# Optimization experiments

Measured on AMD Instinct MI355X. Metric: run time of the kernel, lower is better.

The kernel has to match this reference:

```python
import jax, jax.numpy as jnp
import numpy as np

N, D = 16384, 32          # nodes, max neighbors
IN_F, HID, OUT_F = 128, 128, 128
HEADS = 8
HD = HID // HEADS         # head dim
TDIM = 64                 # Time2Vec dim
NORM = float(np.sqrt(1.0 / HD))


def _lin_params(key, fan_in, fan_out):
    k1, k2 = jax.random.split(key)
    lim = 1.0 / np.sqrt(fan_in)
    W = jax.random.uniform(k1, (fan_in, fan_out), jnp.float32, -lim, lim)
    b = jax.random.uniform(k2, (fan_out,), jnp.float32, -lim, lim)
    return W, b


def setup_inputs() -> dict:
    key = jax.random.key(0)
    ks = jax.random.split(key, 16)
    x = jax.random.normal(ks[0], (N, IN_F), jnp.float32)
    neighbors = jax.random.randint(ks[1], (N, D), 0, N)
    times = jax.random.uniform(ks[2], (N, D), jnp.float32)
    t = jax.random.uniform(ks[3], (1,), jnp.float32)
    # node KQV
    Wk, bk = _lin_params(ks[4], IN_F, HID)
    Wq, bq = _lin_params(ks[5], IN_F, HID)
    Wv, bv = _lin_params(ks[6], IN_F, HID)
    # Time2Vec kernel: [w0*t+b0, sin(t*W + B)] -> TDIM feats
    w0 = jax.random.normal(ks[7], (1,), jnp.float32)
    b0 = jax.random.normal(ks[8], (1,), jnp.float32)
    Wt = jax.random.normal(ks[9], (1, TDIM - 1), jnp.float32)
    Bt = jax.random.normal(ks[10], (TDIM - 1,), jnp.float32)
    # time KQV
    Wtk, btk = _lin_params(ks[11], TDIM, HID)
    Wtq, btq = _lin_params(ks[12], TDIM, HID)
    Wtv, btv = _lin_params(ks[13], TDIM, HID)
    # output MLP
    W1, b1 = _lin_params(ks[14], HID + IN_F, HID)
    W2, b2 = _lin_params(ks[15], HID, OUT_F)
    return dict(x=x, neighbors=neighbors, times=times, t=t,
                Wk=Wk, bk=bk, Wq=Wq, bq=bq, Wv=Wv, bv=bv,
                w0=w0, b0=b0, Wt=Wt, Bt=Bt,
                Wtk=Wtk, btk=btk, Wtq=Wtq, btq=btq, Wtv=Wtv, btv=btv,
                W1=W1, b1=b1, W2=W2, b2=b2)


def _t2v(ts, w0, b0, Wt, Bt):
    # ts: [..., 1] -> [..., TDIM]
    return jnp.concatenate([ts * w0 + b0, jnp.sin(ts @ Wt + Bt)], axis=-1)


def reference(x, neighbors, times, t,
              Wk, bk, Wq, bq, Wv, bv,
              w0, b0, Wt, Bt,
              Wtk, btk, Wtq, btq, Wtv, btv,
              W1, b1, W2, b2):
    t0 = t[0]
    # node-level K/Q/V for all nodes
    k_ = x @ Wk + bk
    q_ = x @ Wq + bq
    v_ = x @ Wv + bv
    # time encodings
    enc_t = _t2v(t.reshape(1, 1), w0, b0, Wt, Bt)          # [1, TDIM]
    tq = enc_t @ Wtq + btq                                  # [1, HID] (same for every target node)
    enc_nb = _t2v(times[..., None], w0, b0, Wt, Bt)        # [N, D, TDIM]
    tk = enc_nb @ Wtk + btk                                 # [N, D, HID]
    tv = enc_nb @ Wtv + btv
    # gather neighbor K/V and add time encodings
    q = q_ + tq                                             # [N, HID]
    k = k_[neighbors] + tk                                  # [N, D, HID]
    v = v_[neighbors] + tv
    # multi-head attention over (time-masked) neighbors
    qh = q.reshape(N, HEADS, HD)
    kh = k.reshape(N, D, HEADS, HD)
    vh = v.reshape(N, D, HEADS, HD)
    scores = jnp.einsum('nhd,nmhd->nhm', qh, kh) * NORM     # [N, H, D]
    mask = times <= t0                                      # [N, D]
    scores = jnp.where(mask[:, None, :], scores, -1e9)
    attn = jax.nn.softmax(scores, axis=-1)
    h = jnp.einsum('nhm,nmhd->nhd', attn, vh).reshape(N, HID)
    # nodes with no valid (time <= t) neighbors output zeros
    h = jnp.where(mask.any(axis=-1)[:, None], h, 0.0)
    # output MLP on [x || h]
    z = jnp.concatenate([x, h], axis=1)
    return jax.nn.relu(z @ W1 + b1) @ W2 + b2
```

## Files before the change

kernel.cpp:

```cpp
#include <hip/hip_runtime.h>
#include <hip/hip_bf16.h>

#define NNODES 16384

typedef unsigned short u16;
typedef unsigned int   u32;
typedef __attribute__((ext_vector_type(8))) short bf16x8;
typedef __attribute__((ext_vector_type(4))) float f32x4;

__device__ __forceinline__ float bfl(u32 u) { return __uint_as_float(u << 16); }
__device__ __forceinline__ float bfh(u32 u) { return __uint_as_float(u & 0xffff0000u); }
__device__ __forceinline__ u16 f2b(float f) {
    u32 u = __float_as_uint(f);
    return (u16)((u + 0x7fffu + ((u >> 16) & 1u)) >> 16);
}
__device__ __forceinline__ u32 pk2(float a, float b) {
    return (u32)f2b(a) | ((u32)f2b(b) << 16);
}
__device__ __forceinline__ bf16x8 bcast8(int4 v) {
    return __builtin_bit_cast(bf16x8, v);
}

#if defined(__has_builtin)
#if __has_builtin(__builtin_amdgcn_fdot2_f32_bf16)
#define HAVE_DOT2 1
#endif
#endif
#ifndef HAVE_DOT2
#define HAVE_DOT2 0
#endif

#if HAVE_DOT2
typedef __attribute__((ext_vector_type(2))) __bf16 bf16x2;
__device__ __forceinline__ float dot2b(u32 a, u32 b, float c) {
    return __builtin_amdgcn_fdot2_f32_bf16(__builtin_bit_cast(bf16x2, a),
                                           __builtin_bit_cast(bf16x2, b), c, false);
}
#else
__device__ __forceinline__ float dot2b(u32 a, u32 b, float c) {
    return c + bfl(a) * bfl(b) + bfh(a) * bfh(b);
}
#endif

__global__ __launch_bounds__(256) void setup_all(
    const float* __restrict__ Wk, const float* __restrict__ Wq,
    const float* __restrict__ Wv, const float* __restrict__ W1,
    const float* __restrict__ W2,
    const float* __restrict__ t,  const float* __restrict__ bq,
    const float* __restrict__ btq,const float* __restrict__ Wtq,
    const float* __restrict__ w0, const float* __restrict__ b0,
    const float* __restrict__ Wt, const float* __restrict__ Bt,
    const float* __restrict__ Wtk,const float* __restrict__ Wtv,
    u16* __restrict__ Wts, float* __restrict__ qbias,
    float* __restrict__ gb, u32* __restrict__ Wtvp, u16* __restrict__ WGt)
{
    __shared__ float sb[128 * 17 + 64 * 17];
    int b = blockIdx.x, tt = threadIdx.x;

    if (b < 96) {
        int mat = b >> 4, tile = b & 15;
        const float* src = (mat == 0) ? Wk : (mat == 1) ? Wq : (mat == 2) ? Wv
                         : (mat == 3) ? W1 : (mat == 4) ? (W1 + 128 * 128) : W2;
        u16* dst = Wts + (size_t)mat * 16384;
        #pragma unroll
        for (int i = 0; i < 4; i++) {
            int o = i * 256 + tt;
            int cl = o >> 7, k = o & 127;
            int c = tile * 8 + cl;
            dst[c * 128 + k] = f2b(src[k * 128 + c]);
        }
    } else if (b == 96 || b == 97) {
        float tv = t[0];
        if (tt < 64)
            sb[tt] = (tt == 0) ? (w0[0] * tv + b0[0])
                               : __sinf(tv * Wt[tt - 1] + Bt[tt - 1]);
        __syncthreads();
        if (tt < 128) {
            float s = bq[tt] + btq[tt];
            for (int k = 0; k < 64; k++)
                s += sb[k] * Wtq[k * 128 + tt];
            sb[64 + tt] = s;
            if (b == 96) qbias[tt] = s;
        }
        __syncthreads();
        if (b == 97) {
            #pragma unroll
            for (int r = 0; r < 2; r++) {
                int hj = tt + r * 256;
                int h = hj >> 6, j = hj & 63;
                float s = 0.f;
                #pragma unroll
                for (int d = 0; d < 16; d++)
                    s += sb[64 + h * 16 + d] * Wtk[(size_t)j * 128 + h * 16 + d];
                gb[hj] = s;
            }
        }
    } else if (b == 98) {
        #pragma unroll
        for (int i = 0; i < 16; i++) {
            int idx = i * 256 + tt;
            int kp = idx >> 7, c = idx & 127;
            Wtvp[idx] = pk2(Wtv[(size_t)(2 * kp) * 128 + c],
                            Wtv[(size_t)(2 * kp + 1) * 128 + c]);
        }
    } else {
        int h = b - 99;
        float* WqL  = sb;
        float* WtkL = sb + 128 * 17;
        #pragma unroll
        for (int i = 0; i < 8; i++) {
            int o = i * 256 + tt;
            int k = o >> 4, d = o & 15;
            WqL[k * 17 + d] = Wq[(size_t)k * 128 + h * 16 + d];
        }
        #pragma unroll
        for (int i = 0; i < 4; i++) {
            int o = i * 256 + tt;
            int j = o >> 4, d = o & 15;
            WtkL[j * 17 + d] = Wtk[(size_t)j * 128 + h * 16 + d];
        }
        __syncthreads();
        int j = tt >> 2, kb = (tt & 3) * 32;
        float wk[16];
        #pragma unroll
        for (int d = 0; d < 16; d++) wk[d] = WtkL[j * 17 + d];
        u32 out[16];
        #pragma unroll
        for (int kk2 = 0; kk2 < 16; kk2++) {
            int k = kb + 2 * kk2;
            float s0 = 0.f, s1 = 0.f;
            #pragma unroll
            for (int d = 0; d < 16; d++) {
                s0 += WqL[k * 17 + d] * wk[d];
                s1 += WqL[(k + 1) * 17 + d] * wk[d];
            }
            out[kk2] = pk2(s0, s1);
        }
        int4* dst = (int4*)(WGt + (size_t)(h * 64 + j) * 128 + kb);
        const int4* srcv = (const int4*)out;
        #pragma unroll
        for (int i = 0; i < 4; i++) dst[i] = srcv[i];
    }
}

__global__ __launch_bounds__(256) void gemm8m2(
    const float* __restrict__ x, const u16* __restrict__ Wts,
    const u16* __restrict__ WGt,
    const float* __restrict__ bk, const float* __restrict__ qbias,
    const float* __restrict__ bv, const float* __restrict__ b1,
    const float* __restrict__ gb,
    u16* __restrict__ Kb, u16* __restrict__ Qb,
    u16* __restrict__ Vb, u16* __restrict__ Pb, u16* __restrict__ Gb)
{
    __shared__ u16 As[128 * 128];
    __shared__ u16 Ws[128 * 128];
    int t = threadIdx.x;
    int rb = blockIdx.x * 128;
    int pair = blockIdx.y;

    u32* As32 = (u32*)As;
    u32* Ws32 = (u32*)Ws;
    const float2* Ap = (const float2*)(x + (size_t)rb * 128);
    #pragma unroll
    for (int i = 0; i < 32; i++) {
        int idx2 = i * 256 + t;
        int r = idx2 >> 6, k2 = idx2 & 63;
        float2 v = Ap[idx2];
        As32[(r * 64 + k2) ^ ((r & 7) << 2)] = pk2(v.x, v.y);
    }

    int wid = t >> 6, lane = t & 63;
    int l15 = lane & 15, lg = lane >> 4;
    int mb = wid * 32;
    int xo = (l15 & 7) << 3;

    #pragma unroll
    for (int half = 0; half < 2; half++) {
        int mat = pair + half * 4;
        const u16* Wt = (mat < 4) ? (Wts + (size_t)mat * 16384)
                                  : (WGt + (size_t)(mat - 4) * 16384);
        const float* bias = (mat == 0) ? bk : (mat == 1) ? qbias
                          : (mat == 2) ? bv : (mat == 3) ? b1
                          : (gb + (mat - 4) * 128);
        const u32* Wp = (const u32*)Wt;
        #pragma unroll
        for (int i = 0; i < 32; i++) {
            int idx2 = i * 256 + t;
            int c = idx2 >> 6, k2 = idx2 & 63;
            Ws32[(c * 64 + k2) ^ ((c & 7) << 2)] = Wp[idx2];
        }
        __syncthreads();

        f32x4 acc[2][8];
        #pragma unroll
        for (int mi = 0; mi < 2; mi++)
            #pragma unroll
            for (int nt = 0; nt < 8; nt++)
                acc[mi][nt] = (f32x4){0.f, 0.f, 0.f, 0.f};

        #pragma unroll
        for (int ks = 0; ks < 4; ks++) {
            int kq = ks * 32 + lg * 8;
            bf16x8 a0 = *(bf16x8*)&As[((mb + l15) * 128 + kq) ^ xo];
            bf16x8 a1 = *(bf16x8*)&As[((mb + 16 + l15) * 128 + kq) ^ xo];
            #pragma unroll
            for (int nt = 0; nt < 8; nt++) {
                bf16x8 b = *(bf16x8*)&Ws[((nt * 16 + l15) * 128 + kq) ^ xo];
                acc[0][nt] = __builtin_amdgcn_mfma_f32_16x16x32_bf16(a0, b, acc[0][nt], 0, 0, 0);
                acc[1][nt] = __builtin_amdgcn_mfma_f32_16x16x32_bf16(a1, b, acc[1][nt], 0, 0, 0);
            }
        }

        u16* dst = (mat == 0) ? Kb : (mat == 1) ? Qb : (mat == 2) ? Vb
                 : (mat == 3) ? Pb : Gb;
        #pragma unroll
        for (int mi = 0; mi < 2; mi++) {
            #pragma unroll
            for (int nt = 0; nt < 8; nt++) {
                int c = nt * 16 + l15;
                float bvv = bias[c];
                #pragma unroll
                for (int j = 0; j < 4; j++) {
                    size_t row = rb + mb + mi * 16 + lg * 4 + j;
                    float v = acc[mi][nt][j] + bvv;
                    if (mat < 4) dst[row * 128 + c] = f2b(v);
                    else         dst[row * 512 + (size_t)(mat - 4) * 128 + c] = f2b(v);
                }
            }
        }
        __syncthreads();
    }
}

__global__ __launch_bounds__(256) void mlp_fused(
    const u16* __restrict__ Hb, const u16* __restrict__ Wts,
    const u16* __restrict__ Pb, const float* __restrict__ b2,
    float* __restrict__ out)
{
    __shared__ u16 As[64 * 128];
    __shared__ u16 Ws[128 * 128];
    int t = threadIdx.x;
    int rb = blockIdx.x * 64;
    u32* As32 = (u32*)As;
    u32* Ws32 = (u32*)Ws;

    const u32* Hp = (const u32*)(Hb + (size_t)rb * 128);
    #pragma unroll
    for (int i = 0; i < 16; i++) {
        int idx2 = i * 256 + t;
        int r = idx2 >> 6, k2 = idx2 & 63;
        As32[(r * 64 + k2) ^ ((r & 7) << 2)] = Hp[idx2];
    }
    {
        const u32* Wp = (const u32*)(Wts + 4 * 16384);
        #pragma unroll
        for (int i = 0; i < 32; i++) {
            int idx2 = i * 256 + t;
            int c = idx2 >> 6, k2 = idx2 & 63;
            Ws32[(c * 64 + k2) ^ ((c & 7) << 2)] = Wp[idx2];
        }
    }
    __syncthreads();

    int wid = t >> 6, lane = t & 63;
    int l15 = lane & 15, lg = lane >> 4;
    int mb = wid * 16;
    int xo = (l15 & 7) << 3;

    f32x4 acc[8];
    #pragma unroll
    for (int nt = 0; nt < 8; nt++) acc[nt] = (f32x4){0.f, 0.f, 0.f, 0.f};
    #pragma unroll
    for (int ks = 0; ks < 4; ks++) {
        int kq = ks * 32 + lg * 8;
        bf16x8 a0 = *(bf16x8*)&As[((mb + l15) * 128 + kq) ^ xo];
        #pragma unroll
        for (int nt = 0; nt < 8; nt++) {
            bf16x8 b = *(bf16x8*)&Ws[((nt * 16 + l15) * 128 + kq) ^ xo];
            acc[nt] = __builtin_amdgcn_mfma_f32_16x16x32_bf16(a0, b, acc[nt], 0, 0, 0);
        }
    }
    __syncthreads();

    #pragma unroll
    for (int nt = 0; nt < 8; nt++) {
        int c = nt * 16 + l15;
        #pragma unroll
        for (int j = 0; j < 4; j++) {
            int row = mb + lg * 4 + j;
            float pv = bfl((u32)Pb[(size_t)(rb + row) * 128 + c]);
            float v = fmaxf(acc[nt][j] + pv, 0.f);
            As[(row * 128 + c) ^ ((row & 7) << 3)] = f2b(v);
        }
    }
    {
        const u32* Wp = (const u32*)(Wts + 5 * 16384);
        #pragma unroll
        for (int i = 0; i < 32; i++) {
            int idx2 = i * 256 + t;
            int c = idx2 >> 6, k2 = idx2 & 63;
            Ws32[(c * 64 + k2) ^ ((c & 7) << 2)] = Wp[idx2];
        }
    }
    __syncthreads();

    #pragma unroll
    for (int nt = 0; nt < 8; nt++) acc[nt] = (f32x4){0.f, 0.f, 0.f, 0.f};
    #pragma unroll
    for (int ks = 0; ks < 4; ks++) {
        int kq = ks * 32 + lg * 8;
        bf16x8 a0 = *(bf16x8*)&As[((mb + l15) * 128 + kq) ^ xo];
        #pragma unroll
        for (int nt = 0; nt < 8; nt++) {
            bf16x8 b = *(bf16x8*)&Ws[((nt * 16 + l15) * 128 + kq) ^ xo];
            acc[nt] = __builtin_amdgcn_mfma_f32_16x16x32_bf16(a0, b, acc[nt], 0, 0, 0);
        }
    }
    #pragma unroll
    for (int nt = 0; nt < 8; nt++) {
        int c = nt * 16 + l15;
        float bvv = b2[c];
        #pragma unroll
        for (int j = 0; j < 4; j++) {
            size_t row = rb + mb + lg * 4 + j;
            out[row * 128 + c] = acc[nt][j] + bvv;
        }
    }
}

__global__ __launch_bounds__(256, 5) void attn_kernel(
    const int*   __restrict__ neighbors, const float* __restrict__ times,
    const float* __restrict__ tptr,
    const u16* __restrict__ Kb, const u16* __restrict__ Qb,
    const u16* __restrict__ Vb, const u16* __restrict__ Gb,
    const float* __restrict__ btk,  const u32* __restrict__ Wtvp,
    const float* __restrict__ btv,
    const float* __restrict__ w0,   const float* __restrict__ b0,
    const float* __restrict__ Wt,   const float* __restrict__ Bt,
    u16* __restrict__ Hb)
{
    __shared__ u16   enc[4][32][72];
    __shared__ u32   gbp[4][8][32];
    __shared__ u32   qb[4][64];
    __shared__ float pbuf[4][8][33];
    __shared__ u16   ewp[4][8][66];
    __shared__ int   nbb[4][32];
    __shared__ float cb_[4][8];

    int t = threadIdx.x;
    int wid = t >> 6, lane = t & 63;
    int n = blockIdx.x * 4 + wid;
    float t0 = tptr[0];
    int l15 = lane & 15, lg = lane >> 4;

    qb[wid][lane] = ((const u32*)Qb)[(size_t)n * 64 + lane];
    {
        int4 g4 = *(const int4*)((const u32*)Gb + (size_t)n * 256 + 4 * lane);
        const u32* gw = (const u32*)&g4;
        #pragma unroll
        for (int i = 0; i < 4; i++) {
            int q4 = 4 * lane + i;
            gbp[wid][q4 >> 5][q4 & 31] = gw[i];
        }
    }

    int m = lane & 31, h2 = lane >> 5;
    if (lane < 32) nbb[wid][lane] = neighbors[n * 32 + lane];
    float tm = times[n * 32 + m];
    bool valid = (tm <= t0);
    unsigned long long bal = __ballot(valid);
    bool anyv = (bal != 0ull);

    u32 vpre[32];
    #pragma unroll
    for (int mm = 0; mm < 32; mm++) {
        int nbm = nbb[wid][mm];
        vpre[mm] = *(const u32*)(Vb + (size_t)nbm * 128 + 2 * lane);
    }

    float W0 = w0[0], B0 = b0[0];
    int kbase = 32 * h2;
    #pragma unroll
    for (int i = 0; i < 16; i++) {
        int k0 = kbase + 2 * i;
        float v0 = (k0 == 0) ? (W0 * tm + B0) : __sinf(tm * Wt[k0 - 1] + Bt[k0 - 1]);
        float v1 = __sinf(tm * Wt[k0] + Bt[k0]);
        *(u32*)&enc[wid][m][k0] = pk2(v0, v1);
    }

    if (lane < 8) {
        float s = 0.f;
        #pragma unroll
        for (int j = 0; j < 8; j++) {
            u32 qp = qb[wid][lane * 8 + j];
            s += bfl(qp) * btk[lane * 16 + 2 * j] + bfh(qp) * btk[lane * 16 + 2 * j + 1];
        }
        cb_[wid][lane] = s;
    }

    f32x4 accS[2];
    accS[0] = (f32x4){0.f, 0.f, 0.f, 0.f};
    accS[1] = (f32x4){0.f, 0.f, 0.f, 0.f};

    int nb0 = nbb[wid][l15];
    int nb1 = nbb[wid][l15 + 16];
    const u16* K0 = Kb + (size_t)nb0 * 128;
    const u16* K1 = Kb + (size_t)nb1 * 128;
    const int4 zero4 = {0, 0, 0, 0};
    #pragma unroll
    for (int ks = 0; ks < 4; ks++) {
        bf16x8 qf = bcast8((l15 == ks * 2 + (lg >> 1))
                               ? *(const int4*)&qb[wid][ks * 16 + lg * 4]
                               : zero4);
        bf16x8 k0f = bcast8(*(const int4*)(K0 + ks * 32 + lg * 8));
        bf16x8 k1f = bcast8(*(const int4*)(K1 + ks * 32 + lg * 8));
        accS[0] = __builtin_amdgcn_mfma_f32_16x16x32_bf16(k0f, qf, accS[0], 0, 0, 0);
        accS[1] = __builtin_amdgcn_mfma_f32_16x16x32_bf16(k1f, qf, accS[1], 0, 0, 0);
    }
    #pragma unroll
    for (int ks = 0; ks < 2; ks++) {
        int4 gi = zero4;
        if (l15 < 8) {
            int2 ga = *(const int2*)&gbp[wid][l15][ks * 16 + lg * 4];
            int2 gbq = *(const int2*)&gbp[wid][l15][ks * 16 + lg * 4 + 2];
            gi.x = ga.x; gi.y = ga.y; gi.z = gbq.x; gi.w = gbq.y;
        }
        bf16x8 gf = bcast8(gi);
        bf16x8 e0 = *(const bf16x8*)&enc[wid][l15][ks * 32 + lg * 8];
        bf16x8 e1 = *(const bf16x8*)&enc[wid][l15 + 16][ks * 32 + lg * 8];
        accS[0] = __builtin_amdgcn_mfma_f32_16x16x32_bf16(e0, gf, accS[0], 0, 0, 0);
        accS[1] = __builtin_amdgcn_mfma_f32_16x16x32_bf16(e1, gf, accS[1], 0, 0, 0);
    }

    float cbv = (l15 < 8) ? cb_[wid][l15] : 0.f;
    float sc[2][4];
    #pragma unroll
    for (int mt = 0; mt < 2; mt++) {
        #pragma unroll
        for (int j = 0; j < 4; j++) {
            int mr = mt * 16 + lg * 4 + j;
            float v = 0.25f * (accS[mt][j] + cbv);
            sc[mt][j] = ((bal >> mr) & 1ull) ? v : -1e9f;
        }
    }
    float mx = sc[0][0];
    #pragma unroll
    for (int mt = 0; mt < 2; mt++)
        #pragma unroll
        for (int j = 0; j < 4; j++) mx = fmaxf(mx, sc[mt][j]);
    mx = fmaxf(mx, __shfl_xor(mx, 16));
    mx = fmaxf(mx, __shfl_xor(mx, 32));
    float p[2][4];
    float s = 0.f;
    #pragma unroll
    for (int mt = 0; mt < 2; mt++)
        #pragma unroll
        for (int j = 0; j < 4; j++) { p[mt][j] = __expf(sc[mt][j] - mx); s += p[mt][j]; }
    s += __shfl_xor(s, 16);
    s += __shfl_xor(s, 32);
    float inv = 1.0f / s;
    if (l15 < 8) {
        #pragma unroll
        for (int mt = 0; mt < 2; mt++)
            #pragma unroll
            for (int j = 0; j < 4; j++)
                pbuf[wid][l15][mt * 16 + lg * 4 + j] = p[mt][j] * inv;
    }

    {
        int hh = l15 & 7;
        float pa[8];
        #pragma unroll
        for (int j = 0; j < 8; j++) pa[j] = pbuf[wid][hh][8 * lg + j];
        int4 ai;
        ai.x = pk2(pa[0], pa[1]); ai.y = pk2(pa[2], pa[3]);
        ai.z = pk2(pa[4], pa[5]); ai.w = pk2(pa[6], pa[7]);
        bf16x8 af = bcast8(ai);
        #pragma unroll
        for (int nt = 0; nt < 4; nt++) {
            int col = nt * 16 + l15;
            int4 bi;
            bi.x = (u32)enc[wid][8 * lg + 0][col] | ((u32)enc[wid][8 * lg + 1][col] << 16);
            bi.y = (u32)enc[wid][8 * lg + 2][col] | ((u32)enc[wid][8 * lg + 3][col] << 16);
            bi.z = (u32)enc[wid][8 * lg + 4][col] | ((u32)enc[wid][8 * lg + 5][col] << 16);
            bi.w = (u32)enc[wid][8 * lg + 6][col] | ((u32)enc[wid][8 * lg + 7][col] << 16);
            bf16x8 bfr = bcast8(bi);
            f32x4 ce = (f32x4){0.f, 0.f, 0.f, 0.f};
            ce = __builtin_amdgcn_mfma_f32_16x16x32_bf16(af, bfr, ce, 0, 0, 0);
            if (lg < 2) {
                #pragma unroll
                for (int j = 0; j < 4; j++)
                    ewp[wid][4 * lg + j][col] = f2b(ce[j]);
            }
        }
    }

    int myh = lane >> 3;
    float av0 = 0.f, av1 = 0.f;
    #pragma unroll
    for (int mm = 0; mm < 32; mm++) {
        float a = pbuf[wid][myh][mm];
        av0 += a * bfl(vpre[mm]);
        av1 += a * bfh(vpre[mm]);
    }
    float ht0 = 0.f, ht1 = 0.f;
    #pragma unroll 8
    for (int kp = 0; kp < 32; kp++) {
        u32 ew = *(const u32*)&ewp[wid][myh][2 * kp];
        int2 wv = *(const int2*)&Wtvp[kp * 128 + 2 * lane];
        ht0 = dot2b(ew, (u32)wv.x, ht0);
        ht1 = dot2b(ew, (u32)wv.y, ht1);
    }
    float2 bt2 = *(const float2*)&btv[2 * lane];
    float ox = anyv ? (av0 + ht0 + bt2.x) : 0.0f;
    float oy = anyv ? (av1 + ht1 + bt2.y) : 0.0f;
    ((u32*)Hb)[(size_t)n * 64 + lane] = pk2(ox, oy);
}

extern "C" void kernel_launch(void* const* d_in, const int* in_sizes, int n_in,
                              void* d_out, int out_size, void* d_ws, size_t ws_size,
                              hipStream_t stream)
{
    const float* x        = (const float*)d_in[0];
    const int*   neighbors= (const int*)  d_in[1];
    const float* times    = (const float*)d_in[2];
    const float* t        = (const float*)d_in[3];
    const float* Wk  = (const float*)d_in[4];
    const float* bk  = (const float*)d_in[5];
    const float* Wq  = (const float*)d_in[6];
    const float* bq  = (const float*)d_in[7];
    const float* Wv  = (const float*)d_in[8];
    const float* bv  = (const float*)d_in[9];
    const float* w0  = (const float*)d_in[10];
    const float* b0  = (const float*)d_in[11];
    const float* Wt  = (const float*)d_in[12];
    const float* Bt  = (const float*)d_in[13];
    const float* Wtk = (const float*)d_in[14];
    const float* btk = (const float*)d_in[15];
    const float* Wtq = (const float*)d_in[16];
    const float* btq = (const float*)d_in[17];
    const float* Wtv = (const float*)d_in[18];
    const float* btv = (const float*)d_in[19];
    const float* W1  = (const float*)d_in[20];
    const float* b1  = (const float*)d_in[21];
    const float* W2  = (const float*)d_in[22];
    const float* b2  = (const float*)d_in[23];

    float* ws = (float*)d_ws;
    const size_t NF = (size_t)NNODES * 128;
    u16*   Kb    = (u16*)ws;
    u16*   Qb    = Kb + NF;
    u16*   Vb    = Qb + NF;
    u16*   Pb    = Vb + NF;
    u16*   Hb    = Pb + NF;
    u16*   Gb    = Hb + NF;
    float* qbias = (float*)(Gb + (size_t)NNODES * 512);
    u16*   Wts   = (u16*)(qbias + 128);
    u16*   WGt   = Wts + 6 * 16384;
    float* gb    = (float*)(WGt + 65536);
    u32*   Wtvp  = (u32*)(gb + 512);

    setup_all<<<107, 256, 0, stream>>>(Wk, Wq, Wv, W1, W2,
                                       t, bq, btq, Wtq, w0, b0, Wt, Bt,
                                       Wtk, Wtv,
                                       Wts, qbias, gb, Wtvp, WGt);

    gemm8m2<<<dim3(NNODES / 128, 4), 256, 0, stream>>>(
        x, Wts, WGt, bk, qbias, bv, b1, gb, Kb, Qb, Vb, Pb, Gb);

    attn_kernel<<<NNODES / 4, 256, 0, stream>>>(neighbors, times, t,
                                                Kb, Qb, Vb, Gb,
                                                btk, Wtvp, btv, w0, b0, Wt, Bt,
                                                Hb);

    mlp_fused<<<NNODES / 64, 256, 0, stream>>>(Hb, Wts, Pb, b2,
                                               (float*)d_out);
}
```

Measured before the change: 110.0 us.

## Prefetch gathered K rows and G into registers early, replace LDS staging with shuffles

Neighbor indices and the per-head bias are now shared through wave shuffles, so the nbb, gbp and cb_ shared buffers are gone. The gathered K rows and the G fragments are loaded into registers up front, before the Time2Vec sin computation, with a sched_barrier so the global gathers overlap that math. s_setprio is raised around the MFMA sections. This should hide gather latency and cut LDS traffic, but it raises register pressure (vpre plus eight int4 of K) under launch_bounds(256,5), which could cause spills.

```diff
diff --git a/kernel.cpp b/kernel.cpp
--- a/kernel.cpp
+++ b/kernel.cpp
@@ -340,45 +340,53 @@
     u16* __restrict__ Hb)
 {
     __shared__ u16   enc[4][32][72];
-    __shared__ u32   gbp[4][8][32];
     __shared__ u32   qb[4][64];
     __shared__ float pbuf[4][8][33];
     __shared__ u16   ewp[4][8][66];
-    __shared__ int   nbb[4][32];
-    __shared__ float cb_[4][8];
 
     int t = threadIdx.x;
     int wid = t >> 6, lane = t & 63;
     int n = blockIdx.x * 4 + wid;
     float t0 = tptr[0];
     int l15 = lane & 15, lg = lane >> 4;
+    int m = lane & 31;
 
     qb[wid][lane] = ((const u32*)Qb)[(size_t)n * 64 + lane];
-    {
-        int4 g4 = *(const int4*)((const u32*)Gb + (size_t)n * 256 + 4 * lane);
-        const u32* gw = (const u32*)&g4;
-        #pragma unroll
-        for (int i = 0; i < 4; i++) {
-            int q4 = 4 * lane + i;
-            gbp[wid][q4 >> 5][q4 & 31] = gw[i];
-        }
-    }
-
-    int m = lane & 31, h2 = lane >> 5;
-    if (lane < 32) nbb[wid][lane] = neighbors[n * 32 + lane];
+
+    int nb = neighbors[n * 32 + m];
     float tm = times[n * 32 + m];
-    bool valid = (tm <= t0);
-    unsigned long long bal = __ballot(valid);
-    bool anyv = (bal != 0ull);
-
+
+    int nb0 = __shfl(nb, l15);
+    int nb1 = __shfl(nb, l15 + 16);
+    const u16* K0 = Kb + (size_t)nb0 * 128;
+    const u16* K1 = Kb + (size_t)nb1 * 128;
+    int4 k0r[4], k1r[4];
+    #pragma unroll
+    for (int ks = 0; ks < 4; ks++) {
+        k0r[ks] = *(const int4*)(K0 + ks * 32 + lg * 8);
+        k1r[ks] = *(const int4*)(K1 + ks * 32 + lg * 8);
+    }
     u32 vpre[32];
     #pragma unroll
     for (int mm = 0; mm < 32; mm++) {
-        int nbm = nbb[wid][mm];
+        int nbm = __shfl(nb, mm);
         vpre[mm] = *(const u32*)(Vb + (size_t)nbm * 128 + 2 * lane);
     }
+    const int4 zero4 = {0, 0, 0, 0};
+    int4 g0i = zero4, g1i = zero4;
+    if (l15 < 8) {
+        const u32* Gr = (const u32*)Gb + (size_t)n * 256 + l15 * 32 + lg * 4;
+        int2 a0 = *(const int2*)(Gr);
+        int2 b0 = *(const int2*)(Gr + 2);
+        int2 a1 = *(const int2*)(Gr + 16);
+        int2 b1 = *(const int2*)(Gr + 18);
+        g0i = (int4){a0.x, a0.y, b0.x, b0.y};
+        g1i = (int4){a1.x, a1.y, b1.x, b1.y};
+    }
+    __builtin_amdgcn_sched_barrier(0);
 
     float W0 = w0[0], B0 = b0[0];
+    int h2 = lane >> 5;
     int kbase = 32 * h2;
     #pragma unroll
     for (int i = 0; i < 16; i++) {
@@ -388,51 +396,47 @@
         *(u32*)&enc[wid][m][k0] = pk2(v0, v1);
     }
 
+    float s_cb = 0.f;
     if (lane < 8) {
-        float s = 0.f;
         #pragma unroll
         for (int j = 0; j < 8; j++) {
             u32 qp = qb[wid][lane * 8 + j];
-            s += bfl(qp) * btk[lane * 16 + 2 * j] + bfh(qp) * btk[lane * 16 + 2 * j + 1];
-        }
-        cb_[wid][lane] = s;
-    }
+            s_cb += bfl(qp) * btk[lane * 16 + 2 * j] + bfh(qp) * btk[lane * 16 + 2 * j + 1];
+        }
+    }
+    float cbv = __shfl(s_cb, l15);
+
+    bool valid = (tm <= t0);
+    unsigned long long bal = __ballot(valid);
+    bool anyv = (bal != 0ull);
 
     f32x4 accS[2];
     accS[0] = (f32x4){0.f, 0.f, 0.f, 0.f};
     accS[1] = (f32x4){0.f, 0.f, 0.f, 0.f};
 
-    int nb0 = nbb[wid][l15];
-    int nb1 = nbb[wid][l15 + 16];
-    const u16* K0 = Kb + (size_t)nb0 * 128;
-    const u16* K1 = Kb + (size_t)nb1 * 128;
-    const int4 zero4 = {0, 0, 0, 0};
+    __builtin_amdgcn_s_setprio(1);
     #pragma unroll
     for (int ks = 0; ks < 4; ks++) {
         bf16x8 qf = bcast8((l15 == ks * 2 + (lg >> 1))
                                ? *(const int4*)&qb[wid][ks * 16 + lg * 4]
                                : zero4);
-        bf16x8 k0f = bcast8(*(const int4*)(K0 + ks * 32 + lg * 8));
-        bf16x8 k1f = bcast8(*(const int4*)(K1 + ks * 32 + lg * 8));
-        accS[0] = __builtin_amdgcn_mfma_f32_16x16x32_bf16(k0f, qf, accS[0], 0, 0, 0);
-        accS[1] = __builtin_amdgcn_mfma_f32_16x16x32_bf16(k1f, qf, accS[1], 0, 0, 0);
-    }
-    #pragma unroll
-    for (int ks = 0; ks < 2; ks++) {
-        int4 gi = zero4;
-        if (l15 < 8) {
-            int2 ga = *(const int2*)&gbp[wid][l15][ks * 16 + lg * 4];
-            int2 gbq = *(const int2*)&gbp[wid][l15][ks * 16 + lg * 4 + 2];
-            gi.x = ga.x; gi.y = ga.y; gi.z = gbq.x; gi.w = gbq.y;
-        }
-        bf16x8 gf = bcast8(gi);
-        bf16x8 e0 = *(const bf16x8*)&enc[wid][l15][ks * 32 + lg * 8];
-        bf16x8 e1 = *(const bf16x8*)&enc[wid][l15 + 16][ks * 32 + lg * 8];
-        accS[0] = __builtin_amdgcn_mfma_f32_16x16x32_bf16(e0, gf, accS[0], 0, 0, 0);
-        accS[1] = __builtin_amdgcn_mfma_f32_16x16x32_bf16(e1, gf, accS[1], 0, 0, 0);
-    }
-
-    float cbv = (l15 < 8) ? cb_[wid][l15] : 0.f;
+        accS[0] = __builtin_amdgcn_mfma_f32_16x16x32_bf16(bcast8(k0r[ks]), qf, accS[0], 0, 0, 0);
+        accS[1] = __builtin_amdgcn_mfma_f32_16x16x32_bf16(bcast8(k1r[ks]), qf, accS[1], 0, 0, 0);
+    }
+    {
+        bf16x8 gf0 = bcast8(g0i);
+        bf16x8 e00 = *(const bf16x8*)&enc[wid][l15][lg * 8];
+        bf16x8 e10 = *(const bf16x8*)&enc[wid][l15 + 16][lg * 8];
+        accS[0] = __builtin_amdgcn_mfma_f32_16x16x32_bf16(e00, gf0, accS[0], 0, 0, 0);
+        accS[1] = __builtin_amdgcn_mfma_f32_16x16x32_bf16(e10, gf0, accS[1], 0, 0, 0);
+        bf16x8 gf1 = bcast8(g1i);
+        bf16x8 e01 = *(const bf16x8*)&enc[wid][l15][32 + lg * 8];
+        bf16x8 e11 = *(const bf16x8*)&enc[wid][l15 + 16][32 + lg * 8];
+        accS[0] = __builtin_amdgcn_mfma_f32_16x16x32_bf16(e01, gf1, accS[0], 0, 0, 0);
+        accS[1] = __builtin_amdgcn_mfma_f32_16x16x32_bf16(e11, gf1, accS[1], 0, 0, 0);
+    }
+    __builtin_amdgcn_s_setprio(0);
+
     float sc[2][4];
     #pragma unroll
     for (int mt = 0; mt < 2; mt++) {
@@ -476,6 +480,7 @@
         ai.x = pk2(pa[0], pa[1]); ai.y = pk2(pa[2], pa[3]);
         ai.z = pk2(pa[4], pa[5]); ai.w = pk2(pa[6], pa[7]);
         bf16x8 af = bcast8(ai);
+        __builtin_amdgcn_s_setprio(1);
         #pragma unroll
         for (int nt = 0; nt < 4; nt++) {
             int col = nt * 16 + l15;
@@ -493,6 +498,7 @@
                     ewp[wid][4 * lg + j][col] = f2b(ce[j]);
             }
         }
+        __builtin_amdgcn_s_setprio(0);
     }
 
     int myh = lane >> 3;
```

After: 137.2 us. +24.7%, slower.

## Shrink row tiles in projection GEMM and output MLP for more blocks

Applied to the files above, without the earlier changes.

The projection GEMM now uses 64-row tiles, and each block handles four weight matrices instead of two, so the grid becomes 256x2 instead of 128x4. The output MLP uses 32-row tiles, with the four waves split as two row halves by two column halves. Both changes raise the number of blocks and cut LDS per block, which should improve occupancy and load balance across CUs. The cost is that each block reloads full weight tiles for fewer rows, so total weight traffic into LDS goes up and each wave does less MFMA work per load.

```diff
diff --git a/kernel.cpp b/kernel.cpp
--- a/kernel.cpp
+++ b/kernel.cpp
@@ -143,7 +143,7 @@
     }
 }
 
-__global__ __launch_bounds__(256) void gemm8m2(
+__global__ __launch_bounds__(256) void gemm8m4(
     const float* __restrict__ x, const u16* __restrict__ Wts,
     const u16* __restrict__ WGt,
     const float* __restrict__ bk, const float* __restrict__ qbias,
@@ -152,17 +152,17 @@
     u16* __restrict__ Kb, u16* __restrict__ Qb,
     u16* __restrict__ Vb, u16* __restrict__ Pb, u16* __restrict__ Gb)
 {
-    __shared__ u16 As[128 * 128];
+    __shared__ u16 As[64 * 128];
     __shared__ u16 Ws[128 * 128];
     int t = threadIdx.x;
-    int rb = blockIdx.x * 128;
-    int pair = blockIdx.y;
+    int rb = blockIdx.x * 64;
+    int grp = blockIdx.y;
 
     u32* As32 = (u32*)As;
     u32* Ws32 = (u32*)Ws;
     const float2* Ap = (const float2*)(x + (size_t)rb * 128);
     #pragma unroll
-    for (int i = 0; i < 32; i++) {
+    for (int i = 0; i < 16; i++) {
         int idx2 = i * 256 + t;
         int r = idx2 >> 6, k2 = idx2 & 63;
         float2 v = Ap[idx2];
@@ -171,18 +171,19 @@
 
     int wid = t >> 6, lane = t & 63;
     int l15 = lane & 15, lg = lane >> 4;
-    int mb = wid * 32;
+    int mb = wid * 16;
     int xo = (l15 & 7) << 3;
 
     #pragma unroll
-    for (int half = 0; half < 2; half++) {
-        int mat = pair + half * 4;
+    for (int mi = 0; mi < 4; mi++) {
+        int mat = grp * 4 + mi;
         const u16* Wt = (mat < 4) ? (Wts + (size_t)mat * 16384)
                                   : (WGt + (size_t)(mat - 4) * 16384);
         const float* bias = (mat == 0) ? bk : (mat == 1) ? qbias
                           : (mat == 2) ? bv : (mat == 3) ? b1
                           : (gb + (mat - 4) * 128);
         const u32* Wp = (const u32*)Wt;
+        __syncthreads();
         #pragma unroll
         for (int i = 0; i < 32; i++) {
             int idx2 = i * 256 + t;
@@ -191,44 +192,34 @@
         }
         __syncthreads();
 
-        f32x4 acc[2][8];
-        #pragma unroll
-        for (int mi = 0; mi < 2; mi++)
-            #pragma unroll
-            for (int nt = 0; nt < 8; nt++)
-                acc[mi][nt] = (f32x4){0.f, 0.f, 0.f, 0.f};
-
+        f32x4 acc[8];
+        #pragma unroll
+        for (int nt = 0; nt < 8; nt++) acc[nt] = (f32x4){0.f, 0.f, 0.f, 0.f};
         #pragma unroll
         for (int ks = 0; ks < 4; ks++) {
             int kq = ks * 32 + lg * 8;
             bf16x8 a0 = *(bf16x8*)&As[((mb + l15) * 128 + kq) ^ xo];
-            bf16x8 a1 = *(bf16x8*)&As[((mb + 16 + l15) * 128 + kq) ^ xo];
             #pragma unroll
             for (int nt = 0; nt < 8; nt++) {
                 bf16x8 b = *(bf16x8*)&Ws[((nt * 16 + l15) * 128 + kq) ^ xo];
-                acc[0][nt] = __builtin_amdgcn_mfma_f32_16x16x32_bf16(a0, b, acc[0][nt], 0, 0, 0);
-                acc[1][nt] = __builtin_amdgcn_mfma_f32_16x16x32_bf16(a1, b, acc[1][nt], 0, 0, 0);
+                acc[nt] = __builtin_amdgcn_mfma_f32_16x16x32_bf16(a0, b, acc[nt], 0, 0, 0);
             }
         }
 
         u16* dst = (mat == 0) ? Kb : (mat == 1) ? Qb : (mat == 2) ? Vb
                  : (mat == 3) ? Pb : Gb;
         #pragma unroll
-        for (int mi = 0; mi < 2; mi++) {
+        for (int nt = 0; nt < 8; nt++) {
+            int c = nt * 16 + l15;
+            float bvv = bias[c];
             #pragma unroll
-            for (int nt = 0; nt < 8; nt++) {
-                int c = nt * 16 + l15;
-                float bvv = bias[c];
-                #pragma unroll
-                for (int j = 0; j < 4; j++) {
-                    size_t row = rb + mb + mi * 16 + lg * 4 + j;
-                    float v = acc[mi][nt][j] + bvv;
-                    if (mat < 4) dst[row * 128 + c] = f2b(v);
-                    else         dst[row * 512 + (size_t)(mat - 4) * 128 + c] = f2b(v);
-                }
+            for (int j = 0; j < 4; j++) {
+                size_t row = rb + mb + lg * 4 + j;
+                float v = acc[nt][j] + bvv;
+                if (mat < 4) dst[row * 128 + c] = f2b(v);
+                else         dst[row * 512 + (size_t)(mat - 4) * 128 + c] = f2b(v);
             }
         }
-        __syncthreads();
     }
 }
 
@@ -237,16 +228,16 @@
     const u16* __restrict__ Pb, const float* __restrict__ b2,
     float* __restrict__ out)
 {
-    __shared__ u16 As[64 * 128];
+    __shared__ u16 As[32 * 128];
     __shared__ u16 Ws[128 * 128];
     int t = threadIdx.x;
-    int rb = blockIdx.x * 64;
+    int rb = blockIdx.x * 32;
     u32* As32 = (u32*)As;
     u32* Ws32 = (u32*)Ws;
 
     const u32* Hp = (const u32*)(Hb + (size_t)rb * 128);
     #pragma unroll
-    for (int i = 0; i < 16; i++) {
+    for (int i = 0; i < 8; i++) {
         int idx2 = i * 256 + t;
         int r = idx2 >> 6, k2 = idx2 & 63;
         As32[(r * 64 + k2) ^ ((r & 7) << 2)] = Hp[idx2];
@@ -264,27 +255,28 @@
 
     int wid = t >> 6, lane = t & 63;
     int l15 = lane & 15, lg = lane >> 4;
-    int mb = wid * 16;
+    int rh = wid >> 1, ch = wid & 1;
+    int mb = rh * 16;
     int xo = (l15 & 7) << 3;
 
-    f32x4 acc[8];
-    #pragma unroll
-    for (int nt = 0; nt < 8; nt++) acc[nt] = (f32x4){0.f, 0.f, 0.f, 0.f};
+    f32x4 acc[4];
+    #pragma unroll
+    for (int nt = 0; nt < 4; nt++) acc[nt] = (f32x4){0.f, 0.f, 0.f, 0.f};
     #pragma unroll
     for (int ks = 0; ks < 4; ks++) {
         int kq = ks * 32 + lg * 8;
         bf16x8 a0 = *(bf16x8*)&As[((mb + l15) * 128 + kq) ^ xo];
         #pragma unroll
-        for (int nt = 0; nt < 8; nt++) {
-            bf16x8 b = *(bf16x8*)&Ws[((nt * 16 + l15) * 128 + kq) ^ xo];
+        for (int nt = 0; nt < 4; nt++) {
+            bf16x8 b = *(bf16x8*)&Ws[(((ch * 4 + nt) * 16 + l15) * 128 + kq) ^ xo];
             acc[nt] = __builtin_amdgcn_mfma_f32_16x16x32_bf16(a0, b, acc[nt], 0, 0, 0);
         }
     }
     __syncthreads();
 
     #pragma unroll
-    for (int nt = 0; nt < 8; nt++) {
-        int c = nt * 16 + l15;
+    for (int nt = 0; nt < 4; nt++) {
+        int c = ch * 64 + nt * 16 + l15;
         #pragma unroll
         for (int j = 0; j < 4; j++) {
             int row = mb + lg * 4 + j;
@@ -305,20 +297,20 @@
     __syncthreads();
 
     #pragma unroll
-    for (int nt = 0; nt < 8; nt++) acc[nt] = (f32x4){0.f, 0.f, 0.f, 0.f};
+    for (int nt = 0; nt < 4; nt++) acc[nt] = (f32x4){0.f, 0.f, 0.f, 0.f};
     #pragma unroll
     for (int ks = 0; ks < 4; ks++) {
         int kq = ks * 32 + lg * 8;
         bf16x8 a0 = *(bf16x8*)&As[((mb + l15) * 128 + kq) ^ xo];
         #pragma unroll
-        for (int nt = 0; nt < 8; nt++) {
-            bf16x8 b = *(bf16x8*)&Ws[((nt * 16 + l15) * 128 + kq) ^ xo];
+        for (int nt = 0; nt < 4; nt++) {
+            bf16x8 b = *(bf16x8*)&Ws[(((ch * 4 + nt) * 16 + l15) * 128 + kq) ^ xo];
             acc[nt] = __builtin_amdgcn_mfma_f32_16x16x32_bf16(a0, b, acc[nt], 0, 0, 0);
         }
     }
     #pragma unroll
-    for (int nt = 0; nt < 8; nt++) {
-        int c = nt * 16 + l15;
+    for (int nt = 0; nt < 4; nt++) {
+        int c = ch * 64 + nt * 16 + l15;
         float bvv = b2[c];
         #pragma unroll
         for (int j = 0; j < 4; j++) {
@@ -565,7 +557,7 @@
                                        Wtk, Wtv,
                                        Wts, qbias, gb, Wtvp, WGt);
 
-    gemm8m2<<<dim3(NNODES / 128, 4), 256, 0, stream>>>(
+    gemm8m4<<<dim3(NNODES / 64, 2), 256, 0, stream>>>(
         x, Wts, WGt, bk, qbias, bv, b1, gb, Kb, Qb, Vb, Pb, Gb);
 
     attn_kernel<<<NNODES / 4, 256, 0, stream>>>(neighbors, times, t,
@@ -573,6 +565,6 @@
                                                 btk, Wtvp, btv, w0, b0, Wt, Bt,
                                                 Hb);
 
-    mlp_fused<<<NNODES / 64, 256, 0, stream>>>(Hb, Wts, Pb, b2,
+    mlp_fused<<<NNODES / 32, 256, 0, stream>>>(Hb, Wts, Pb, b2,
                                                (float*)d_out);
 }
```

Result: faster. 101.3 us (-7.9%).
